# Optimization experiments

Measured on AMD Instinct MI355X. Metric: run time of the kernel, lower is better.

The kernel has to match this reference:

```python
import math
import jax, jax.numpy as jnp
import numpy as np

NUM_BUCKETS = 32
MAX_DISTANCE = 128
N_HEADS = 16
D_KV = 64


def _relative_position_bucket(rel_pos):
    # encoder (bidirectional) path of UMT5Attention._relative_position_bucket
    num_buckets = NUM_BUCKETS // 2
    rel_buckets = (rel_pos > 0).astype(jnp.int32) * num_buckets
    rel_pos = jnp.abs(rel_pos)
    max_exact = num_buckets // 2
    is_small = rel_pos < max_exact
    # clamp to 1 inside log only to avoid nan; those entries are masked by is_small
    rel_pos_large = max_exact + (
        jnp.log(jnp.maximum(rel_pos, 1).astype(jnp.float32) / max_exact)
        / math.log(MAX_DISTANCE / max_exact)
        * (num_buckets - max_exact)
    ).astype(jnp.int32)
    rel_pos_large = jnp.minimum(rel_pos_large, num_buckets - 1)
    return rel_buckets + jnp.where(is_small, rel_pos, rel_pos_large)


def compute_bias(rel_bias, q_len, k_len):
    ctx = jnp.arange(q_len, dtype=jnp.int32)[:, None]
    mem = jnp.arange(k_len, dtype=jnp.int32)[None, :]
    bkt = _relative_position_bucket(mem - ctx)          # [q, k]
    values = rel_bias[bkt]                               # [q, k, H]
    return jnp.transpose(values, (2, 0, 1))[None]        # [1, H, q, k]


def setup_inputs() -> dict:
    key = jax.random.key(0)
    ks = jax.random.split(key, 6)
    B, S, D = 2, 2048, 1024
    s = 1.0 / math.sqrt(D)
    return {
        "hidden_states": jax.random.normal(ks[0], (B, S, D), jnp.float32),
        "attention_mask": jnp.ones((B, S), jnp.int32),
        "Wq": jax.random.normal(ks[1], (D, D), jnp.float32) * s,
        "Wk": jax.random.normal(ks[2], (D, D), jnp.float32) * s,
        "Wv": jax.random.normal(ks[3], (D, D), jnp.float32) * s,
        "Wo": jax.random.normal(ks[4], (D, D), jnp.float32) * s,
        "rel_bias": jax.random.normal(ks[5], (NUM_BUCKETS, N_HEADS), jnp.float32),
    }


def reference(hidden_states, attention_mask, Wq, Wk, Wv, Wo, rel_bias):
    b, s, _ = hidden_states.shape
    n, c = N_HEADS, D_KV
    q = (hidden_states @ Wq).reshape(b, s, n, c)
    k = (hidden_states @ Wk).reshape(b, s, n, c)
    v = (hidden_states @ Wv).reshape(b, s, n, c)
    position_bias = compute_bias(rel_bias, s, s)          # [1, H, s, s]
    mask = attention_mask[:, None, None, :]               # [b, 1, 1, s]
    position_bias = jnp.where(mask == 0,
                              jnp.finfo(hidden_states.dtype).min,
                              position_bias)
    # T5-style: no 1/sqrt(d) query scaling
    attn = jnp.einsum('binc,bjnc->bnij', q, k) + position_bias
    attn = jax.nn.softmax(attn, axis=-1)
    o = jnp.einsum('bnij,bjnc->binc', attn, v).reshape(b, s, n * c)
    return o @ Wo
```

## Files before the change

### kernel.cpp

```cpp
#include <hip/hip_runtime.h>
#include <hip/hip_bf16.h>

#define NH 16
#define DC 64
#define SEQ 2048
#define BATCH 2
#define DM 1024
#define MTOT (BATCH*SEQ)

#define LOG2E 1.44269504f
#define SMAX_BOUND 48.0f

typedef unsigned short u16;
typedef unsigned int u32;
typedef __bf16 bf16x8 __attribute__((ext_vector_type(8)));
typedef float f32x4 __attribute__((ext_vector_type(4)));
typedef int i32x4 __attribute__((ext_vector_type(4)));
typedef unsigned u32x2v __attribute__((ext_vector_type(2)));

struct __attribute__((packed, aligned(4))) f4u { f32x4 v; };

__device__ __forceinline__ u16 f2bf(float f) {
    unsigned int x = __float_as_uint(f);
    unsigned int r = (x + 0x7fffu + ((x >> 16) & 1u)) >> 16;
    return (u16)r;
}
__device__ __forceinline__ u32 cvtpk(float a, float b) {
    u32 r;
    asm("v_cvt_pk_bf16_f32 %0, %1, %2" : "=v"(r) : "v"(a), "v"(b));
    return r;
}

__device__ __forceinline__ f32x4 mfma16(bf16x8 a, bf16x8 b, f32x4 c) {
    return __builtin_amdgcn_mfma_f32_16x16x32_bf16(a, b, c, 0, 0, 0);
}

__device__ __forceinline__ void glds(const u16* g, u16* l) {
    __builtin_amdgcn_global_load_lds(
        (const __attribute__((address_space(1))) void*)g,
        (__attribute__((address_space(3))) void*)l, 16, 0, 0);
}

__device__ __forceinline__ float psum32(float v) {
    u32x2v t = __builtin_amdgcn_permlane32_swap(__float_as_uint(v), __float_as_uint(v), false, false);
    return __uint_as_float(t.x) + __uint_as_float(t.y);
}
__device__ __forceinline__ float psum16(float v) {
    u32x2v t = __builtin_amdgcn_permlane16_swap(__float_as_uint(v), __float_as_uint(v), false, false);
    return __uint_as_float(t.x) + __uint_as_float(t.y);
}


__global__ void convert_hs(const float* __restrict__ src, u16* __restrict__ dst, int n4) {
    int idx = blockIdx.x * blockDim.x + threadIdx.x;
    int stride = gridDim.x * blockDim.x;
    for (int i = idx; i < n4; i += stride) {
        float4 v = reinterpret_cast<const float4*>(src)[i];
        uint2 o;
        o.x = (unsigned)f2bf(v.x) | ((unsigned)f2bf(v.y) << 16);
        o.y = (unsigned)f2bf(v.z) | ((unsigned)f2bf(v.w) << 16);
        reinterpret_cast<uint2*>(dst)[i] = o;
    }
}

__global__ void wtrans(const float* __restrict__ Wq, const float* __restrict__ Wk,
                       const float* __restrict__ Wv, const float* __restrict__ Wo,
                       u16* __restrict__ wT) {
    int z = blockIdx.z;
    const float* W = (z == 0) ? Wq : (z == 1) ? Wk : (z == 2) ? Wv : Wo;
    float sc = (z == 0) ? LOG2E : 1.0f;
    u16* WT = wT + (size_t)z * DM * DM;
    __shared__ float tile[32][33];
    int tx = threadIdx.x, ty = threadIdx.y;
    int kbase = blockIdx.y * 32, nbase = blockIdx.x * 32;
#pragma unroll
    for (int i = 0; i < 4; i++)
        tile[ty * 4 + i][tx] = W[(size_t)(kbase + ty * 4 + i) * DM + nbase + tx];
    __syncthreads();
#pragma unroll
    for (int i = 0; i < 4; i++)
        WT[(size_t)(nbase + ty * 4 + i) * DM + kbase + tx] = f2bf(tile[tx][ty * 4 + i] * sc);
}

__global__ void bias_table(const float* __restrict__ rel_bias, float* __restrict__ tab) {
    int idx = blockIdx.x * blockDim.x + threadIdx.x;
    if (idx >= NH * 2 * SEQ) return;
    int n = idx >> 12;
    int dpos = idx & 4095;
    int delta = dpos - 2048;
    int rb = (delta > 0) ? 16 : 0;
    int a = (delta < 0) ? -delta : delta;
    int ib;
    if (a < 8) {
        ib = a;
    } else {
        ib = 8 + (int)(logf((float)a / 8.0f) / logf(16.0f) * 8.0f);
        if (ib > 15) ib = 15;
    }
    tab[idx] = (rel_bias[(rb + ib) * NH + n] - SMAX_BOUND) * LOG2E;
}

__global__ __launch_bounds__(256) void vtrans(const u16* __restrict__ V, u16* __restrict__ VT) {
    int st = blockIdx.x;
    int hb = blockIdx.y;
    const u16* src = V + ((size_t)hb * SEQ + st * 64) * DC;
    u16* dst = VT + (size_t)hb * DC * SEQ + st * 64;
    __shared__ u16 t[64][65];
    int tid = threadIdx.x;
    int r = tid >> 2, c0 = (tid & 3) * 16;
    union { bf16x8 v; u16 s[8]; } a0, a1;
    a0.v = *reinterpret_cast<const bf16x8*>(src + (size_t)r * DC + c0);
    a1.v = *reinterpret_cast<const bf16x8*>(src + (size_t)r * DC + c0 + 8);
#pragma unroll
    for (int j = 0; j < 8; j++) { t[r][c0 + j] = a0.s[j]; t[r][c0 + 8 + j] = a1.s[j]; }
    __syncthreads();
    int c = tid >> 2, s0 = (tid & 3) * 16;
    union { bf16x8 v; u16 s[8]; } o0, o1;
#pragma unroll
    for (int j = 0; j < 8; j++) { o0.s[j] = t[s0 + j][c]; o1.s[j] = t[s0 + 8 + j][c]; }
    *reinterpret_cast<bf16x8*>(dst + (size_t)c * SEQ + s0)     = o0.v;
    *reinterpret_cast<bf16x8*>(dst + (size_t)c * SEQ + s0 + 8) = o1.v;
}


template<int MODE>
__global__ __launch_bounds__(256) void gemm_bt(
    const u16* __restrict__ A, const u16* __restrict__ BT,
    u16* __restrict__ qkvout, float* __restrict__ fout)
{
    const int NTILES = DM / 128;
    const int MTILES = MTOT / 128;
    __shared__ u16 As[128 * 32];
    __shared__ u16 Bs[128 * 32];

    int nb8 = gridDim.x >> 3;
    int bid = (blockIdx.x & 7) * nb8 + (blockIdx.x >> 3);

    int proj = 0, mt, nt;
    if (MODE == 0) {
        proj = bid / (MTILES * NTILES);
        int r = bid % (MTILES * NTILES);
        mt = r / NTILES; nt = r % NTILES;
    } else {
        mt = bid / NTILES; nt = bid % NTILES;
    }
    const u16* Bp = BT + (size_t)proj * DM * DM;
    int m0 = mt * 128, n0 = nt * 128;
    int tid = threadIdx.x;
    int lane = tid & 63, wid = tid >> 6;
    int wrow = (wid >> 1) * 64, wcol = (wid & 1) * 64;

    f32x4 acc[4][4] = {};

    int srow = lane >> 2;
    int skoff = (lane & 3) * 8;

    for (int k0 = 0; k0 < DM; k0 += 32) {
        __syncthreads();
#pragma unroll
        for (int t = 0; t < 2; t++) {
            int chunk = wid * 2 + t;
            int row = chunk * 16 + srow;
            glds(A + (size_t)(m0 + row) * DM + k0 + skoff, &As[chunk * 512]);
        }
#pragma unroll
        for (int t = 0; t < 2; t++) {
            int chunk = wid * 2 + t;
            int row = chunk * 16 + srow;
            glds(Bp + (size_t)(n0 + row) * DM + k0 + skoff, &Bs[chunk * 512]);
        }
        __syncthreads();

        int ko = (lane >> 4) * 8;
        bf16x8 af[4], bfr[4];
#pragma unroll
        for (int mi = 0; mi < 4; mi++)
            af[mi] = *reinterpret_cast<const bf16x8*>(&As[(wrow + mi * 16 + (lane & 15)) * 32 + ko]);
#pragma unroll
        for (int ni = 0; ni < 4; ni++)
            bfr[ni] = *reinterpret_cast<const bf16x8*>(&Bs[(wcol + ni * 16 + (lane & 15)) * 32 + ko]);
#pragma unroll
        for (int mi = 0; mi < 4; mi++)
#pragma unroll
            for (int ni = 0; ni < 4; ni++)
                acc[mi][ni] = mfma16(af[mi], bfr[ni], acc[mi][ni]);
    }

    int rbase = (lane >> 4) * 4;
    int cidx = lane & 15;
#pragma unroll
    for (int mi = 0; mi < 4; mi++) {
#pragma unroll
        for (int ni = 0; ni < 4; ni++) {
#pragma unroll
            for (int r = 0; r < 4; r++) {
                int gm = m0 + wrow + mi * 16 + rbase + r;
                int gn = n0 + wcol + ni * 16 + cidx;
                float v = acc[mi][ni][r];
                if (MODE == 0) {
                    int b = gm >> 11, s = gm & (SEQ - 1);
                    int h = gn >> 6, c = gn & 63;
                    size_t off = (((size_t)b * NH + h) * SEQ + s) * DC + c;
                    qkvout[(size_t)proj * MTOT * DM + off] = f2bf(v);
                } else {
                    fout[(size_t)gm * DM + gn] = v;
                }
            }
        }
    }
}


__global__ __launch_bounds__(256) void attn_kernel(
    const u16* __restrict__ Q, const u16* __restrict__ K, const u16* __restrict__ VT,
    const int* __restrict__ mask, const float* __restrict__ btab,
    u16* __restrict__ O)
{
    __shared__ u16 smem[16384];

    int wg = blockIdx.x;
    int sw = (wg & 7) * 128 + (wg >> 3);
    int qt = sw & 31;
    int bh = sw >> 5;
    int h = bh & 15, b = bh >> 4;

    int tid = threadIdx.x, lane = tid & 63, wid = tid >> 6;
    int q15 = lane & 15, hi = lane >> 4;

    const u16* Qp  = Q  + (((size_t)b * NH + h) * SEQ) * DC;
    const u16* Kp  = K  + (((size_t)b * NH + h) * SEQ) * DC;
    const u16* VTp = VT + ((size_t)b * NH + h) * DC * SEQ;

    int iq = qt * 64 + wid * 16 + q15;

    bf16x8 qf0 = *reinterpret_cast<const bf16x8*>(Qp + (size_t)iq * DC + hi * 8);
    bf16x8 qf1 = *reinterpret_cast<const bf16x8*>(Qp + (size_t)iq * DC + 32 + hi * 8);

    int n0 = (wid * 2 + 0) * 64 + lane;
    int n1 = (wid * 2 + 1) * 64 + lane;
    int rA = n0 >> 3, rB = n1 >> 3;
    const u16* gK0 = Kp  + (size_t)rA * DC + (((n0 & 7) ^ (rA & 7)) * 8);
    const u16* gK1 = Kp  + (size_t)rB * DC + (((n1 & 7) ^ (rB & 7)) * 8);
    const u16* gV0 = VTp + (size_t)rA * SEQ + (((n0 & 7) ^ (rA & 7)) * 8);
    const u16* gV1 = VTp + (size_t)rB * SEQ + (((n1 & 7) ^ (rB & 7)) * 8);

    int x0 = (hi)     ^ (q15 & 7);
    int x1 = (hi + 4) ^ (q15 & 7);

    const float* bp = btab + (size_t)h * 2 * SEQ + 2048 + hi * 4 - iq;
    const int* mkp = mask + (size_t)b * SEQ + hi * 4;

    float l_part = 0.0f;
    f32x4 oacc[4] = {};

    glds(gK0, &smem[(wid * 2 + 0) * 512]);
    glds(gK1, &smem[(wid * 2 + 1) * 512]);
    glds(gV0, &smem[4096 + (wid * 2 + 0) * 512]);
    glds(gV1, &smem[4096 + (wid * 2 + 1) * 512]);

#pragma unroll 1
    for (int t = 0; t < SEQ / 64; t++) {
        u16* KsT = smem + ((t & 1) << 13);
        u16* VsT = KsT + 4096;
        int kt = t * 64;

        f32x4 bv4[4]; i32x4 mv4[4];
#pragma unroll
        for (int kf = 0; kf < 4; kf++) {
            bv4[kf] = reinterpret_cast<const f4u*>(bp + kt + kf * 16)->v;
            mv4[kf] = *reinterpret_cast<const i32x4*>(mkp + kt + kf * 16);
        }

        if (t < SEQ / 64 - 1) {
            u16* KsN = smem + (((t + 1) & 1) << 13);
            int aK = (t + 1) * 64 * DC;
            int aV = (t + 1) * 64;
            glds(gK0 + aK, &KsN[(wid * 2 + 0) * 512]);
            glds(gK1 + aK, &KsN[(wid * 2 + 1) * 512]);
            glds(gV0 + aV, &KsN[4096 + (wid * 2 + 0) * 512]);
            glds(gV1 + aV, &KsN[4096 + (wid * 2 + 1) * 512]);
            asm volatile("s_waitcnt vmcnt(12)" ::: "memory");
        } else {
            asm volatile("s_waitcnt vmcnt(8)" ::: "memory");
        }
        asm volatile("s_barrier" ::: "memory");

        f32x4 s[4];
#pragma unroll
        for (int kf = 0; kf < 4; kf++) {
            bf16x8 ka0 = *reinterpret_cast<const bf16x8*>(&KsT[(kf * 16 + q15) * 64 + x0 * 8]);
            bf16x8 ka1 = *reinterpret_cast<const bf16x8*>(&KsT[(kf * 16 + q15) * 64 + x1 * 8]);
            f32x4 z = {};
            z = mfma16(ka0, qf0, z);
            z = mfma16(ka1, qf1, z);
            s[kf] = z;
        }

#pragma unroll
        for (int kf = 0; kf < 4; kf++) {
#pragma unroll
            for (int r = 0; r < 4; r++) {
                float sv = s[kf][r] + ((mv4[kf][r] != 0) ? bv4[kf][r] : -1e30f);
                float p = exp2f(sv);
                s[kf][r] = p;
                l_part += p;
            }
        }

        u32 c00 = cvtpk(s[0][0], s[0][1]);
        u32 c01 = cvtpk(s[0][2], s[0][3]);
        u32 c10 = cvtpk(s[1][0], s[1][1]);
        u32 c11 = cvtpk(s[1][2], s[1][3]);
        u32 c20 = cvtpk(s[2][0], s[2][1]);
        u32 c21 = cvtpk(s[2][2], s[2][3]);
        u32 c30 = cvtpk(s[3][0], s[3][1]);
        u32 c31 = cvtpk(s[3][2], s[3][3]);
        {
            u32x2v t0 = __builtin_amdgcn_permlane32_swap(c00, c10, false, false); c00 = t0.x; c10 = t0.y;
            u32x2v t1 = __builtin_amdgcn_permlane32_swap(c01, c11, false, false); c01 = t1.x; c11 = t1.y;
            u32x2v t2 = __builtin_amdgcn_permlane32_swap(c20, c30, false, false); c20 = t2.x; c30 = t2.y;
            u32x2v t3 = __builtin_amdgcn_permlane32_swap(c21, c31, false, false); c21 = t3.x; c31 = t3.y;
            u32x2v t4 = __builtin_amdgcn_permlane16_swap(c00, c10, false, false); c00 = t4.x; c10 = t4.y;
            u32x2v t5 = __builtin_amdgcn_permlane16_swap(c01, c11, false, false); c01 = t5.x; c11 = t5.y;
            u32x2v t6 = __builtin_amdgcn_permlane16_swap(c20, c30, false, false); c20 = t6.x; c30 = t6.y;
            u32x2v t7 = __builtin_amdgcn_permlane16_swap(c21, c31, false, false); c21 = t7.x; c31 = t7.y;
        }
        union { u32 w[4]; bf16x8 v; } up0, up1;
        up0.w[0] = c00; up0.w[1] = c01; up0.w[2] = c10; up0.w[3] = c11;
        up1.w[0] = c20; up1.w[1] = c21; up1.w[2] = c30; up1.w[3] = c31;
        bf16x8 pa0 = up0.v;
        bf16x8 pa1 = up1.v;

#pragma unroll
        for (int ci = 0; ci < 4; ci++) {
            bf16x8 v0 = *reinterpret_cast<const bf16x8*>(&VsT[(ci * 16 + q15) * 64 + x0 * 8]);
            bf16x8 v1 = *reinterpret_cast<const bf16x8*>(&VsT[(ci * 16 + q15) * 64 + x1 * 8]);
            oacc[ci] = mfma16(v0, pa0, oacc[ci]);
            oacc[ci] = mfma16(v1, pa1, oacc[ci]);
        }

        asm volatile("s_barrier" ::: "memory");
    }

    float l_tot = psum16(psum32(l_part));
    float rl = 1.0f / l_tot;
    __syncthreads();
    u16* Ot = smem;
#pragma unroll
    for (int ci = 0; ci < 4; ci++) {
        u32 w0 = cvtpk(oacc[ci][0] * rl, oacc[ci][1] * rl);
        u32 w1 = cvtpk(oacc[ci][2] * rl, oacc[ci][3] * rl);
        int base = (wid * 16 + q15) * 72 + ci * 16 + hi * 4;
        *reinterpret_cast<u32*>(&Ot[base])     = w0;
        *reinterpret_cast<u32*>(&Ot[base + 2]) = w1;
    }
    __syncthreads();
    int row = tid >> 2, part = tid & 3;
    bf16x8 o0 = *reinterpret_cast<const bf16x8*>(&Ot[row * 72 + part * 16]);
    bf16x8 o1 = *reinterpret_cast<const bf16x8*>(&Ot[row * 72 + part * 16 + 8]);
    size_t ob = ((size_t)b * SEQ + qt * 64 + row) * DM + h * DC + part * 16;
    *reinterpret_cast<bf16x8*>(&O[ob])     = o0;
    *reinterpret_cast<bf16x8*>(&O[ob + 8]) = o1;
}


extern "C" void kernel_launch(void* const* d_in, const int* in_sizes, int n_in,
                              void* d_out, int out_size, void* d_ws, size_t ws_size,
                              hipStream_t stream) {
    const float* hs   = (const float*)d_in[0];
    const int*   mask = (const int*)d_in[1];
    const float* Wq   = (const float*)d_in[2];
    const float* Wk   = (const float*)d_in[3];
    const float* Wv   = (const float*)d_in[4];
    const float* Wo   = (const float*)d_in[5];
    const float* rb   = (const float*)d_in[6];

    char* ws = (char*)d_ws;
    u16* hsb  = (u16*)(ws);
    u16* wT   = (u16*)(ws + 8388608);
    u16* Qb   = (u16*)(ws + 16777216);
    u16* Ob   = (u16*)(ws + 41943040);
    float* btab = (float*)(ws + 50331648);
    float* out = (float*)d_out;

    u16* VT = hsb;

    convert_hs<<<2048, 256, 0, stream>>>(hs, hsb, MTOT * DM / 4);
    wtrans<<<dim3(32, 32, 4), dim3(32, 8), 0, stream>>>(Wq, Wk, Wv, Wo, wT);
    bias_table<<<256, 256, 0, stream>>>(rb, btab);
    gemm_bt<0><<<768, 256, 0, stream>>>(hsb, wT, Qb, nullptr);
    vtrans<<<dim3(32, 32), 256, 0, stream>>>(Qb + 2 * (size_t)MTOT * DM, VT);
    attn_kernel<<<1024, 256, 0, stream>>>(
        Qb, Qb + (size_t)MTOT * DM, VT, mask, btab, Ob);
    gemm_bt<1><<<256, 256, 0, stream>>>(Ob, wT + 3 * (size_t)DM * DM, nullptr, out);
}
```

Baseline: 160.8 us.

## Process two 16-row query tiles per wave to reuse K/V tiles in attention

Each wave now handles 32 query rows (two 16-row sub-tiles) instead of 16, so every K and V fragment loaded from LDS feeds twice as many MFMAs and each workgroup covers 128 queries. The grid is halved to 512 workgroups and the output epilogue is widened to match. The aim is to halve K/V global-to-LDS traffic and LDS reads per query. The waitcnt values are adjusted for the extra loads, and s_setprio raises wave priority around the MFMA blocks. The trade-off is higher register pressure and fewer workgroups (512) on a large GPU, which can lower occupancy and latency hiding.

```diff
diff --git a/kernel.cpp b/kernel.cpp
--- a/kernel.cpp
+++ b/kernel.cpp
@@ -219,9 +219,9 @@
     __shared__ u16 smem[16384];
 
     int wg = blockIdx.x;
-    int sw = (wg & 7) * 128 + (wg >> 3);
-    int qt = sw & 31;
-    int bh = sw >> 5;
+    int sw = (wg & 7) * 64 + (wg >> 3);
+    int qt = sw & 15;
+    int bh = sw >> 4;
     int h = bh & 15, b = bh >> 4;
 
     int tid = threadIdx.x, lane = tid & 63, wid = tid >> 6;
@@ -231,10 +231,14 @@
     const u16* Kp  = K  + (((size_t)b * NH + h) * SEQ) * DC;
     const u16* VTp = VT + ((size_t)b * NH + h) * DC * SEQ;
 
-    int iq = qt * 64 + wid * 16 + q15;
-
-    bf16x8 qf0 = *reinterpret_cast<const bf16x8*>(Qp + (size_t)iq * DC + hi * 8);
-    bf16x8 qf1 = *reinterpret_cast<const bf16x8*>(Qp + (size_t)iq * DC + 32 + hi * 8);
+    int qb = qt * 128 + wid * 32;
+    int iq0 = qb + q15;
+    int iq1 = qb + 16 + q15;
+
+    bf16x8 qf00 = *reinterpret_cast<const bf16x8*>(Qp + (size_t)iq0 * DC + hi * 8);
+    bf16x8 qf01 = *reinterpret_cast<const bf16x8*>(Qp + (size_t)iq0 * DC + 32 + hi * 8);
+    bf16x8 qf10 = *reinterpret_cast<const bf16x8*>(Qp + (size_t)iq1 * DC + hi * 8);
+    bf16x8 qf11 = *reinterpret_cast<const bf16x8*>(Qp + (size_t)iq1 * DC + 32 + hi * 8);
 
     int n0 = (wid * 2 + 0) * 64 + lane;
     int n1 = (wid * 2 + 1) * 64 + lane;
@@ -247,11 +251,12 @@
     int x0 = (hi)     ^ (q15 & 7);
     int x1 = (hi + 4) ^ (q15 & 7);
 
-    const float* bp = btab + (size_t)h * 2 * SEQ + 2048 + hi * 4 - iq;
+    const float* bp0 = btab + (size_t)h * 2 * SEQ + 2048 + hi * 4 - iq0;
+    const float* bp1 = bp0 - 16;
     const int* mkp = mask + (size_t)b * SEQ + hi * 4;
 
-    float l_part = 0.0f;
-    f32x4 oacc[4] = {};
+    float l0 = 0.0f, l1 = 0.0f;
+    f32x4 oacc[4][2] = {};
 
     glds(gK0, &smem[(wid * 2 + 0) * 512]);
     glds(gK1, &smem[(wid * 2 + 1) * 512]);
@@ -264,10 +269,11 @@
         u16* VsT = KsT + 4096;
         int kt = t * 64;
 
-        f32x4 bv4[4]; i32x4 mv4[4];
+        f32x4 bv0[4], bv1[4]; i32x4 mv4[4];
 #pragma unroll
         for (int kf = 0; kf < 4; kf++) {
-            bv4[kf] = reinterpret_cast<const f4u*>(bp + kt + kf * 16)->v;
+            bv0[kf] = reinterpret_cast<const f4u*>(bp0 + kt + kf * 16)->v;
+            bv1[kf] = reinterpret_cast<const f4u*>(bp1 + kt + kf * 16)->v;
             mv4[kf] = *reinterpret_cast<const i32x4*>(mkp + kt + kf * 16);
         }
 
@@ -279,43 +285,53 @@
             glds(gK1 + aK, &KsN[(wid * 2 + 1) * 512]);
             glds(gV0 + aV, &KsN[4096 + (wid * 2 + 0) * 512]);
             glds(gV1 + aV, &KsN[4096 + (wid * 2 + 1) * 512]);
-            asm volatile("s_waitcnt vmcnt(12)" ::: "memory");
+            asm volatile("s_waitcnt vmcnt(4)" ::: "memory");
         } else {
-            asm volatile("s_waitcnt vmcnt(8)" ::: "memory");
+            asm volatile("s_waitcnt vmcnt(0)" ::: "memory");
         }
         asm volatile("s_barrier" ::: "memory");
 
-        f32x4 s[4];
+        f32x4 s0[4], s1[4];
+        __builtin_amdgcn_s_setprio(1);
 #pragma unroll
         for (int kf = 0; kf < 4; kf++) {
             bf16x8 ka0 = *reinterpret_cast<const bf16x8*>(&KsT[(kf * 16 + q15) * 64 + x0 * 8]);
             bf16x8 ka1 = *reinterpret_cast<const bf16x8*>(&KsT[(kf * 16 + q15) * 64 + x1 * 8]);
-            f32x4 z = {};
-            z = mfma16(ka0, qf0, z);
-            z = mfma16(ka1, qf1, z);
-            s[kf] = z;
-        }
+            f32x4 z0 = {};
+            z0 = mfma16(ka0, qf00, z0);
+            z0 = mfma16(ka1, qf01, z0);
+            s0[kf] = z0;
+            f32x4 z1 = {};
+            z1 = mfma16(ka0, qf10, z1);
+            z1 = mfma16(ka1, qf11, z1);
+            s1[kf] = z1;
+        }
+        __builtin_amdgcn_s_setprio(0);
 
 #pragma unroll
         for (int kf = 0; kf < 4; kf++) {
 #pragma unroll
             for (int r = 0; r < 4; r++) {
-                float sv = s[kf][r] + ((mv4[kf][r] != 0) ? bv4[kf][r] : -1e30f);
-                float p = exp2f(sv);
-                s[kf][r] = p;
-                l_part += p;
+                bool mv = (mv4[kf][r] != 0);
+                float sv0 = s0[kf][r] + (mv ? bv0[kf][r] : -1e30f);
+                float sv1 = s1[kf][r] + (mv ? bv1[kf][r] : -1e30f);
+                float p0 = exp2f(sv0);
+                float p1 = exp2f(sv1);
+                s0[kf][r] = p0; l0 += p0;
+                s1[kf][r] = p1; l1 += p1;
             }
         }
 
-        u32 c00 = cvtpk(s[0][0], s[0][1]);
-        u32 c01 = cvtpk(s[0][2], s[0][3]);
-        u32 c10 = cvtpk(s[1][0], s[1][1]);
-        u32 c11 = cvtpk(s[1][2], s[1][3]);
-        u32 c20 = cvtpk(s[2][0], s[2][1]);
-        u32 c21 = cvtpk(s[2][2], s[2][3]);
-        u32 c30 = cvtpk(s[3][0], s[3][1]);
-        u32 c31 = cvtpk(s[3][2], s[3][3]);
+        bf16x8 pa00, pa01, pa10, pa11;
         {
+            u32 c00 = cvtpk(s0[0][0], s0[0][1]);
+            u32 c01 = cvtpk(s0[0][2], s0[0][3]);
+            u32 c10 = cvtpk(s0[1][0], s0[1][1]);
+            u32 c11 = cvtpk(s0[1][2], s0[1][3]);
+            u32 c20 = cvtpk(s0[2][0], s0[2][1]);
+            u32 c21 = cvtpk(s0[2][2], s0[2][3]);
+            u32 c30 = cvtpk(s0[3][0], s0[3][1]);
+            u32 c31 = cvtpk(s0[3][2], s0[3][3]);
             u32x2v t0 = __builtin_amdgcn_permlane32_swap(c00, c10, false, false); c00 = t0.x; c10 = t0.y;
             u32x2v t1 = __builtin_amdgcn_permlane32_swap(c01, c11, false, false); c01 = t1.x; c11 = t1.y;
             u32x2v t2 = __builtin_amdgcn_permlane32_swap(c20, c30, false, false); c20 = t2.x; c30 = t2.y;
@@ -324,43 +340,77 @@
             u32x2v t5 = __builtin_amdgcn_permlane16_swap(c01, c11, false, false); c01 = t5.x; c11 = t5.y;
             u32x2v t6 = __builtin_amdgcn_permlane16_swap(c20, c30, false, false); c20 = t6.x; c30 = t6.y;
             u32x2v t7 = __builtin_amdgcn_permlane16_swap(c21, c31, false, false); c21 = t7.x; c31 = t7.y;
-        }
-        union { u32 w[4]; bf16x8 v; } up0, up1;
-        up0.w[0] = c00; up0.w[1] = c01; up0.w[2] = c10; up0.w[3] = c11;
-        up1.w[0] = c20; up1.w[1] = c21; up1.w[2] = c30; up1.w[3] = c31;
-        bf16x8 pa0 = up0.v;
-        bf16x8 pa1 = up1.v;
-
+            union { u32 w[4]; bf16x8 v; } up0, up1;
+            up0.w[0] = c00; up0.w[1] = c01; up0.w[2] = c10; up0.w[3] = c11;
+            up1.w[0] = c20; up1.w[1] = c21; up1.w[2] = c30; up1.w[3] = c31;
+            pa00 = up0.v; pa01 = up1.v;
+        }
+        {
+            u32 c00 = cvtpk(s1[0][0], s1[0][1]);
+            u32 c01 = cvtpk(s1[0][2], s1[0][3]);
+            u32 c10 = cvtpk(s1[1][0], s1[1][1]);
+            u32 c11 = cvtpk(s1[1][2], s1[1][3]);
+            u32 c20 = cvtpk(s1[2][0], s1[2][1]);
+            u32 c21 = cvtpk(s1[2][2], s1[2][3]);
+            u32 c30 = cvtpk(s1[3][0], s1[3][1]);
+            u32 c31 = cvtpk(s1[3][2], s1[3][3]);
+            u32x2v t0 = __builtin_amdgcn_permlane32_swap(c00, c10, false, false); c00 = t0.x; c10 = t0.y;
+            u32x2v t1 = __builtin_amdgcn_permlane32_swap(c01, c11, false, false); c01 = t1.x; c11 = t1.y;
+            u32x2v t2 = __builtin_amdgcn_permlane32_swap(c20, c30, false, false); c20 = t2.x; c30 = t2.y;
+            u32x2v t3 = __builtin_amdgcn_permlane32_swap(c21, c31, false, false); c21 = t3.x; c31 = t3.y;
+            u32x2v t4 = __builtin_amdgcn_permlane16_swap(c00, c10, false, false); c00 = t4.x; c10 = t4.y;
+            u32x2v t5 = __builtin_amdgcn_permlane16_swap(c01, c11, false, false); c01 = t5.x; c11 = t5.y;
+            u32x2v t6 = __builtin_amdgcn_permlane16_swap(c20, c30, false, false); c20 = t6.x; c30 = t6.y;
+            u32x2v t7 = __builtin_amdgcn_permlane16_swap(c21, c31, false, false); c21 = t7.x; c31 = t7.y;
+            union { u32 w[4]; bf16x8 v; } up0, up1;
+            up0.w[0] = c00; up0.w[1] = c01; up0.w[2] = c10; up0.w[3] = c11;
+            up1.w[0] = c20; up1.w[1] = c21; up1.w[2] = c30; up1.w[3] = c31;
+            pa10 = up0.v; pa11 = up1.v;
+        }
+
+        __builtin_amdgcn_s_setprio(1);
 #pragma unroll
         for (int ci = 0; ci < 4; ci++) {
             bf16x8 v0 = *reinterpret_cast<const bf16x8*>(&VsT[(ci * 16 + q15) * 64 + x0 * 8]);
             bf16x8 v1 = *reinterpret_cast<const bf16x8*>(&VsT[(ci * 16 + q15) * 64 + x1 * 8]);
-            oacc[ci] = mfma16(v0, pa0, oacc[ci]);
-            oacc[ci] = mfma16(v1, pa1, oacc[ci]);
-        }
+            oacc[ci][0] = mfma16(v0, pa00, oacc[ci][0]);
+            oacc[ci][0] = mfma16(v1, pa01, oacc[ci][0]);
+            oacc[ci][1] = mfma16(v0, pa10, oacc[ci][1]);
+            oacc[ci][1] = mfma16(v1, pa11, oacc[ci][1]);
+        }
+        __builtin_amdgcn_s_setprio(0);
 
         asm volatile("s_barrier" ::: "memory");
     }
 
-    float l_tot = psum16(psum32(l_part));
-    float rl = 1.0f / l_tot;
+    float rl0 = 1.0f / psum16(psum32(l0));
+    float rl1 = 1.0f / psum16(psum32(l1));
     __syncthreads();
     u16* Ot = smem;
 #pragma unroll
     for (int ci = 0; ci < 4; ci++) {
-        u32 w0 = cvtpk(oacc[ci][0] * rl, oacc[ci][1] * rl);
-        u32 w1 = cvtpk(oacc[ci][2] * rl, oacc[ci][3] * rl);
-        int base = (wid * 16 + q15) * 72 + ci * 16 + hi * 4;
-        *reinterpret_cast<u32*>(&Ot[base])     = w0;
-        *reinterpret_cast<u32*>(&Ot[base + 2]) = w1;
+        u32 w00 = cvtpk(oacc[ci][0][0] * rl0, oacc[ci][0][1] * rl0);
+        u32 w01 = cvtpk(oacc[ci][0][2] * rl0, oacc[ci][0][3] * rl0);
+        int base0 = (wid * 32 + q15) * 72 + ci * 16 + hi * 4;
+        *reinterpret_cast<u32*>(&Ot[base0])     = w00;
+        *reinterpret_cast<u32*>(&Ot[base0 + 2]) = w01;
+        u32 w10 = cvtpk(oacc[ci][1][0] * rl1, oacc[ci][1][1] * rl1);
+        u32 w11 = cvtpk(oacc[ci][1][2] * rl1, oacc[ci][1][3] * rl1);
+        int base1 = (wid * 32 + 16 + q15) * 72 + ci * 16 + hi * 4;
+        *reinterpret_cast<u32*>(&Ot[base1])     = w10;
+        *reinterpret_cast<u32*>(&Ot[base1 + 2]) = w11;
     }
     __syncthreads();
-    int row = tid >> 2, part = tid & 3;
-    bf16x8 o0 = *reinterpret_cast<const bf16x8*>(&Ot[row * 72 + part * 16]);
-    bf16x8 o1 = *reinterpret_cast<const bf16x8*>(&Ot[row * 72 + part * 16 + 8]);
-    size_t ob = ((size_t)b * SEQ + qt * 64 + row) * DM + h * DC + part * 16;
-    *reinterpret_cast<bf16x8*>(&O[ob])     = o0;
-    *reinterpret_cast<bf16x8*>(&O[ob + 8]) = o1;
+    int row = tid >> 1, part = tid & 1;
+    bf16x8 o0 = *reinterpret_cast<const bf16x8*>(&Ot[row * 72 + part * 32]);
+    bf16x8 o1 = *reinterpret_cast<const bf16x8*>(&Ot[row * 72 + part * 32 + 8]);
+    bf16x8 o2 = *reinterpret_cast<const bf16x8*>(&Ot[row * 72 + part * 32 + 16]);
+    bf16x8 o3 = *reinterpret_cast<const bf16x8*>(&Ot[row * 72 + part * 32 + 24]);
+    size_t ob = ((size_t)b * SEQ + qt * 128 + row) * DM + h * DC + part * 32;
+    *reinterpret_cast<bf16x8*>(&O[ob])      = o0;
+    *reinterpret_cast<bf16x8*>(&O[ob + 8])  = o1;
+    *reinterpret_cast<bf16x8*>(&O[ob + 16]) = o2;
+    *reinterpret_cast<bf16x8*>(&O[ob + 24]) = o3;
 }
 
 
@@ -390,7 +440,7 @@
     bias_table<<<256, 256, 0, stream>>>(rb, btab);
     gemm_bt<0><<<768, 256, 0, stream>>>(hsb, wT, Qb, nullptr);
     vtrans<<<dim3(32, 32), 256, 0, stream>>>(Qb + 2 * (size_t)MTOT * DM, VT);
-    attn_kernel<<<1024, 256, 0, stream>>>(
+    attn_kernel<<<512, 256, 0, stream>>>(
         Qb, Qb + (size_t)MTOT * DM, VT, mask, btab, Ob);
     gemm_bt<1><<<256, 256, 0, stream>>>(Ob, wT + 3 * (size_t)DM * DM, nullptr, out);
 }
```

Result: faster. 149.4 us (-7.1%).
